# Optimization experiments

Hardware: AMD Instinct MI355X
Metric: run time of the kernel (lower is better)

The kernel has to match this reference:

```python
import jax, jax.numpy as jnp
import numpy as np

B, S, M, D, H = 2, 2048, 512, 1024, 16
HD = D // H      # head dim 64
KVC = D // 16    # MLA kv compression dim 64
QC = D // 32     # MLA q compression dim 32
RD = HD          # retrieval (qk) head dim 64
LOOKBACK = 8     # cross_window
EPS = 1e-6


def rmsnorm(x, w):
    return x * jax.lax.rsqrt(jnp.mean(x * x, axis=-1, keepdims=True) + EPS) * w


def setup_inputs():
    key = jax.random.key(0)
    ks = jax.random.split(key, 20)
    g = lambda i, shape: jax.random.normal(ks[i], shape, jnp.float32) * 0.02
    return {
        "x": jax.random.normal(ks[0], (B, S, D), jnp.float32),
        "memory": jax.random.normal(ks[1], (B, M, D), jnp.float32),
        "seg_ids": jnp.sort(jax.random.randint(ks[2], (B, S), 0, M), axis=-1),
        "norm1_w": jnp.ones((D,), jnp.float32),
        "W_dq": g(3, (D, QC)),
        "W_uq": g(4, (QC, H * RD)),
        "W_dkv": g(5, (D, KVC)),
        "W_uk": g(6, (KVC, H * RD)),
        "W_uv": g(7, (KVC, H * HD)),
        "W_o_self": g(8, (H * HD, D)),
        "norm2_w": jnp.ones((D,), jnp.float32),
        "W_q_c": g(9, (D, D)),
        "W_k_c": g(10, (D, D)),
        "W_v_c": g(11, (D, D)),
        "W_o_c": g(12, (D, D)),
        "norm3_w": jnp.ones((D,), jnp.float32),
        "W_gate": g(13, (D, 4 * D)),
        "W_up": g(14, (D, 4 * D)),
        "W_down": g(15, (4 * D, D)),
    }


def reference(x, memory, seg_ids, norm1_w, W_dq, W_uq, W_dkv, W_uk, W_uv,
              W_o_self, norm2_w, W_q_c, W_k_c, W_v_c, W_o_c, norm3_w,
              W_gate, W_up, W_down):
    # ---- MLA causal self-attention (low-rank compressed q/kv) ----
    h = rmsnorm(x, norm1_w)
    q = ((h @ W_dq) @ W_uq).reshape(B, S, H, RD)
    c_kv = h @ W_dkv                                  # [B,S,KVC]
    k = (c_kv @ W_uk).reshape(B, S, H, RD)
    v = (c_kv @ W_uv).reshape(B, S, H, HD)
    scores = jnp.einsum('bihd,bjhd->bhij', q, k) / np.float32(np.sqrt(RD))
    causal = jnp.tril(jnp.ones((S, S), bool))
    scores = jnp.where(causal, scores, -jnp.inf)
    attn = jax.nn.softmax(scores, axis=-1)
    o = jnp.einsum('bhij,bjhd->bihd', attn, v).reshape(B, S, H * HD)
    x = x + o @ W_o_self
    # ---- segment sliding-window cross-attention ----
    h = rmsnorm(x, norm2_w)
    qc = (h @ W_q_c).reshape(B, S, H, HD)
    kc = (memory @ W_k_c).reshape(B, M, H, HD)
    vc = (memory @ W_v_c).reshape(B, M, H, HD)
    sc = jnp.einsum('bihd,bjhd->bhij', qc, kc) / np.float32(np.sqrt(HD))
    kv_pos = jnp.arange(M)
    seg = seg_ids[:, :, None]                          # [B,S,1]
    allowed = (kv_pos[None, None, :] <= seg) & (kv_pos[None, None, :] >= seg - LOOKBACK)
    sc = jnp.where(allowed[:, None, :, :], sc, -jnp.inf)
    ac = jax.nn.softmax(sc, axis=-1)
    oc = jnp.einsum('bhij,bjhd->bihd', ac, vc).reshape(B, S, D)
    x = x + oc @ W_o_c
    # ---- SwiGLU FFN ----
    h = rmsnorm(x, norm3_w)
    x = x + (jax.nn.silu(h @ W_gate) * (h @ W_up)) @ W_down
    return x
```

## Files before the change

### kernel.cpp

```cpp
#include <hip/hip_runtime.h>
#include <stdint.h>

typedef unsigned short U16;
typedef __bf16 bf16x8 __attribute__((ext_vector_type(8)));
typedef unsigned short us8 __attribute__((ext_vector_type(8)));
typedef float f32x4 __attribute__((ext_vector_type(4)));

__device__ __forceinline__ U16 f2bf(float f) {
    unsigned u = __builtin_bit_cast(unsigned, f);
    unsigned r = (u + 0x7fff + ((u >> 16) & 1)) >> 16;
    return (U16)r;
}
__device__ __forceinline__ U16 f2bf_fast(float f) {
    return (U16)((__builtin_bit_cast(unsigned, f) + 0x8000u) >> 16);
}
__device__ __forceinline__ float bf2f(U16 v) {
    return __builtin_bit_cast(float, (unsigned)v << 16);
}
__device__ __forceinline__ bf16x8 ld8(const U16* p) { return __builtin_bit_cast(bf16x8, *(const us8*)p); }

__device__ __forceinline__ void async16(const U16* g, U16* l) {
    auto* gp = (const __attribute__((address_space(1))) U16*)g;
    auto* lp = (__attribute__((address_space(3))) U16*)(uintptr_t)(uint32_t)(uintptr_t)l;
    __builtin_amdgcn_global_load_lds(gp, lp, 16, 0, 0);
}

struct WEnt { const float* src; U16* dst; int K, N, Kpad, Npad, koff, noff, tiles; };
struct WTable { WEnt e[13]; };

__global__ __launch_bounds__(256) void wtrans_all(WTable t) {
    int bx = blockIdx.x, ei = 0;
    while (bx >= t.e[ei].tiles) { bx -= t.e[ei].tiles; ei++; }
    const WEnt E = t.e[ei];
    const int ntn = E.Npad >> 5;
    const int n0 = (bx % ntn) * 32, k0 = (bx / ntn) * 32;
    __shared__ float tile[32][33];
    const int tx = threadIdx.x & 31, ty = threadIdx.x >> 5;
#pragma unroll
    for (int i = 0; i < 4; i++) {
        int kk = k0 + ty + i * 8, n = n0 + tx;
        int k = kk - E.koff;
        float v = (k >= 0 && k < E.K && n < E.N) ? E.src[(size_t)k * E.N + n] : 0.f;
        tile[ty + i * 8][tx] = v;
    }
    __syncthreads();
#pragma unroll
    for (int i = 0; i < 4; i++) {
        int n = n0 + ty + i * 8, kk = k0 + tx;
        E.dst[(size_t)(E.noff + n) * E.Kpad + kk] = f2bf(tile[tx][ty + i * 8]);
    }
}

__global__ __launch_bounds__(256) void f2bf_k(const float* __restrict__ in, U16* __restrict__ out, int n) {
    int i = (blockIdx.x * 256 + threadIdx.x) * 4;
    if (i < n) {
        float4 v = *(const float4*)(in + i);
        out[i + 0] = f2bf(v.x); out[i + 1] = f2bf(v.y);
        out[i + 2] = f2bf(v.z); out[i + 3] = f2bf(v.w);
    }
}

__global__ __launch_bounds__(256) void cq_reduce(const float* __restrict__ p, U16* __restrict__ out) {
    int i = (blockIdx.x * 256 + threadIdx.x) * 4;
    const float4 a = *(const float4*)(p + i);
    const float4 b = *(const float4*)(p + 524288 + i);
    const float4 c = *(const float4*)(p + 2 * 524288 + i);
    const float4 d = *(const float4*)(p + 3 * 524288 + i);
    out[i + 0] = f2bf(a.x + b.x + c.x + d.x);
    out[i + 1] = f2bf(a.y + b.y + c.y + d.y);
    out[i + 2] = f2bf(a.z + b.z + c.z + d.z);
    out[i + 3] = f2bf(a.w + b.w + c.w + d.w);
}

__global__ __launch_bounds__(256) void rmsnorm_k(const float* __restrict__ x, const float* __restrict__ w,
                                                 U16* __restrict__ h) {
    const int row = blockIdx.x, tid = threadIdx.x;
    const float4 v = *(const float4*)(x + (size_t)row * 1024 + tid * 4);
    float ss = v.x * v.x + v.y * v.y + v.z * v.z + v.w * v.w;
#pragma unroll
    for (int o = 32; o > 0; o >>= 1) ss += __shfl_xor(ss, o);
    __shared__ float red[4];
    if ((tid & 63) == 0) red[tid >> 6] = ss;
    __syncthreads();
    float tot = red[0] + red[1] + red[2] + red[3];
    float sc = rsqrtf(tot * (1.0f / 1024.0f) + 1e-6f);
    const float4 wv = *(const float4*)(w + tid * 4);
    U16* hp = h + (size_t)row * 1024 + tid * 4;
    hp[0] = f2bf(v.x * sc * wv.x); hp[1] = f2bf(v.y * sc * wv.y);
    hp[2] = f2bf(v.z * sc * wv.z); hp[3] = f2bf(v.w * sc * wv.w);
}

__global__ __launch_bounds__(256) void qkuv_gemm(const U16* __restrict__ A, const U16* __restrict__ Wuqk,
                                                 const U16* __restrict__ Wuv,
                                                 U16* __restrict__ qkb, U16* __restrict__ vt) {
    __shared__ __align__(16) U16 As[2][128 * 32];
    __shared__ __align__(16) U16 Bs[2][128 * 32];
    __shared__ __align__(16) U16 Ts[4][64 * 80];
    const int tid = threadIdx.x;
    const bool isuv = blockIdx.x >= 16;
    const U16* Bt = isuv ? Wuv : Wuqk;
    const int n0 = (isuv ? blockIdx.x - 16 : blockIdx.x) * 128;
    const int m0 = blockIdx.y * 128;
    const int wave = tid >> 6, lane = tid & 63, l16 = lane & 15, quad = lane >> 4;
    const int wm = (wave >> 1) * 64, wn = (wave & 1) * 64;
    const int sr = lane >> 2, sc = (lane & 3) * 8;
    const U16* gA = A + (size_t)(m0 + wave * 32 + sr) * 128 + sc;
    const U16* gB = Bt + (size_t)(n0 + wave * 32 + sr) * 128 + sc;
    f32x4 acc[4][4] = {};
    for (int kt = 0; kt < 128; kt += 64) {
        __syncthreads();
#pragma unroll
        for (int p = 0; p < 2; p++) {
            const int o = kt + p * 32;
            async16(gA + o, &As[p][(wave * 32) * 32]);
            async16(gA + 16 * 128 + o, &As[p][(wave * 32 + 16) * 32]);
            async16(gB + o, &Bs[p][(wave * 32) * 32]);
            async16(gB + 16 * 128 + o, &Bs[p][(wave * 32 + 16) * 32]);
        }
        __syncthreads();
#pragma unroll
        for (int p = 0; p < 2; p++) {
            bf16x8 af[4], bfr[4];
#pragma unroll
            for (int i = 0; i < 4; i++) {
                af[i]  = ld8(&As[p][(wm + i * 16 + l16) * 32 + quad * 8]);
                bfr[i] = ld8(&Bs[p][(wn + i * 16 + l16) * 32 + quad * 8]);
            }
#pragma unroll
            for (int mi = 0; mi < 4; mi++)
#pragma unroll
                for (int ni = 0; ni < 4; ni++)
                    acc[mi][ni] = __builtin_amdgcn_mfma_f32_16x16x32_bf16(af[mi], bfr[ni], acc[mi][ni], 0, 0, 0);
        }
    }
    if (isuv) {
        U16* T = Ts[wave];
#pragma unroll
        for (int mi = 0; mi < 4; mi++)
#pragma unroll
            for (int ni = 0; ni < 4; ni++)
#pragma unroll
                for (int r = 0; r < 4; r++)
                    T[(ni * 16 + l16) * 80 + mi * 16 + quad * 4 + r] = f2bf(acc[mi][ni][r]);
#pragma unroll
        for (int c = 0; c < 8; c++) {
            int nloc = (lane >> 3) + 8 * c, mloc = (lane & 7) * 8;
            us8 v = *(const us8*)&T[nloc * 80 + mloc];
            *(us8*)&vt[(size_t)(n0 + wn + nloc) * 4096 + (m0 + wm + mloc)] = v;
        }
    } else {
#pragma unroll
        for (int mi = 0; mi < 4; mi++)
#pragma unroll
            for (int r = 0; r < 4; r++) {
                int m = m0 + wm + mi * 16 + quad * 4 + r;
#pragma unroll
                for (int ni = 0; ni < 4; ni++)
                    qkb[(size_t)m * 2048 + n0 + wn + ni * 16 + l16] = f2bf(acc[mi][ni][r]);
            }
    }
}

template <int EPI>
__global__ __launch_bounds__(256) void gemm_m64(const U16* __restrict__ A, const U16* __restrict__ Bt,
                                                void* __restrict__ Cout, const float* __restrict__ resid,
                                                int M, int N, int K, int lda, int ldb, int ldc) {
    __shared__ __align__(16) U16 As[4][64 * 32];
    __shared__ __align__(16) U16 Bs[4][128 * 32];
    const int tid = threadIdx.x;
    const int m0 = blockIdx.y * 64, n0 = blockIdx.x * 128;
    const int k0 = blockIdx.z * K;
    const int wave = tid >> 6, lane = tid & 63, l16 = lane & 15, quad = lane >> 4;
    const int wm = (wave >> 1) * 32, wn = (wave & 1) * 64;
    const int sr = lane >> 2, sc = (lane & 3) * 8;
    const U16* gA = A + (size_t)(m0 + wave * 16 + sr) * lda + sc + k0;
    const U16* gB = Bt + (size_t)(n0 + wave * 32 + sr) * ldb + sc + k0;
    f32x4 acc[2][4] = {};
    for (int kt = 0; kt < K; kt += 128) {
        __syncthreads();
#pragma unroll
        for (int p = 0; p < 4; p++) {
            const int o = kt + p * 32;
            async16(gA + o, &As[p][(wave * 16) * 32]);
            async16(gB + o, &Bs[p][(wave * 32) * 32]);
            async16(gB + (size_t)16 * ldb + o, &Bs[p][(wave * 32 + 16) * 32]);
        }
        __syncthreads();
#pragma unroll
        for (int p = 0; p < 4; p++) {
            bf16x8 af[2], bfr[4];
#pragma unroll
            for (int i = 0; i < 2; i++)
                af[i] = ld8(&As[p][(wm + i * 16 + l16) * 32 + quad * 8]);
#pragma unroll
            for (int i = 0; i < 4; i++)
                bfr[i] = ld8(&Bs[p][(wn + i * 16 + l16) * 32 + quad * 8]);
#pragma unroll
            for (int mi = 0; mi < 2; mi++)
#pragma unroll
                for (int ni = 0; ni < 4; ni++)
                    acc[mi][ni] = __builtin_amdgcn_mfma_f32_16x16x32_bf16(af[mi], bfr[ni], acc[mi][ni], 0, 0, 0);
        }
    }
#pragma unroll
    for (int mi = 0; mi < 2; mi++) {
#pragma unroll
        for (int r = 0; r < 4; r++) {
            int m = m0 + wm + mi * 16 + quad * 4 + r;
#pragma unroll
            for (int ni = 0; ni < 4; ni++) {
                int n = n0 + wn + ni * 16 + l16;
                float val = acc[mi][ni][r];
                if (EPI == 0) ((U16*)Cout)[(size_t)m * ldc + n] = f2bf(val);
                else if (EPI == 1) ((float*)Cout)[(size_t)m * ldc + n] = resid[(size_t)m * ldc + n] + val;
                else if (EPI == 5) ((float*)Cout)[(size_t)blockIdx.z * 524288 + (size_t)m * ldc + n] = val;
            }
        }
    }
}

__global__ __launch_bounds__(256) void qckv_gemm(const U16* __restrict__ hbuf, const U16* __restrict__ Wqc,
                                                 const U16* __restrict__ memb, const U16* __restrict__ Wkvc,
                                                 U16* __restrict__ qcb, U16* __restrict__ kvcb) {
    __shared__ __align__(16) U16 As[4][64 * 32];
    __shared__ __align__(16) U16 Bs[4][128 * 32];
    const int tid = threadIdx.x, bid = blockIdx.x;
    const U16 *A, *Bt; U16* C; int m0, n0, ldc;
    if (bid < 512) { A = hbuf; Bt = Wqc;  C = qcb;  m0 = (bid >> 3) * 64; n0 = (bid & 7) * 128;  ldc = 1024; }
    else { int b2 = bid - 512; A = memb; Bt = Wkvc; C = kvcb; m0 = (b2 >> 4) * 64; n0 = (b2 & 15) * 128; ldc = 2048; }
    const int wave = tid >> 6, lane = tid & 63, l16 = lane & 15, quad = lane >> 4;
    const int wm = (wave >> 1) * 32, wn = (wave & 1) * 64;
    const int sr = lane >> 2, sc = (lane & 3) * 8;
    const U16* gA = A + (size_t)(m0 + wave * 16 + sr) * 1024 + sc;
    const U16* gB = Bt + (size_t)(n0 + wave * 32 + sr) * 1024 + sc;
    f32x4 acc[2][4] = {};
    for (int kt = 0; kt < 1024; kt += 128) {
        __syncthreads();
#pragma unroll
        for (int p = 0; p < 4; p++) {
            const int o = kt + p * 32;
            async16(gA + o, &As[p][(wave * 16) * 32]);
            async16(gB + o, &Bs[p][(wave * 32) * 32]);
            async16(gB + 16 * 1024 + o, &Bs[p][(wave * 32 + 16) * 32]);
        }
        __syncthreads();
#pragma unroll
        for (int p = 0; p < 4; p++) {
            bf16x8 af[2], bfr[4];
#pragma unroll
            for (int i = 0; i < 2; i++)
                af[i] = ld8(&As[p][(wm + i * 16 + l16) * 32 + quad * 8]);
#pragma unroll
            for (int i = 0; i < 4; i++)
                bfr[i] = ld8(&Bs[p][(wn + i * 16 + l16) * 32 + quad * 8]);
#pragma unroll
            for (int mi = 0; mi < 2; mi++)
#pragma unroll
                for (int ni = 0; ni < 4; ni++)
                    acc[mi][ni] = __builtin_amdgcn_mfma_f32_16x16x32_bf16(af[mi], bfr[ni], acc[mi][ni], 0, 0, 0);
        }
    }
#pragma unroll
    for (int mi = 0; mi < 2; mi++)
#pragma unroll
        for (int r = 0; r < 4; r++) {
            int m = m0 + wm + mi * 16 + quad * 4 + r;
#pragma unroll
            for (int ni = 0; ni < 4; ni++)
                C[(size_t)m * ldc + n0 + wn + ni * 16 + l16] = f2bf(acc[mi][ni][r]);
        }
}

__global__ __launch_bounds__(512, 2) void ffn1_8ph(const U16* __restrict__ A, const U16* __restrict__ Wgu,
                                                   U16* __restrict__ Cout) {
    __shared__ __align__(16) U16 As[2][256 * 64];
    __shared__ __align__(16) U16 Bs[2][256 * 64];
    const int tid = threadIdx.x;
    const int wid = tid >> 6, lane = tid & 63;
    const int l16 = lane & 15, quad = lane >> 4;
    const int n0 = blockIdx.x * 128;
    const int m0 = blockIdx.y * 256;
    const int wr = wid >> 2, wc = wid & 3;
    const int wm = wr * 128;
    const int wn = wc * 64;
    const int srow = lane >> 3;
    const int schunk = (lane & 7) ^ srow;
    const U16* gA = A + (size_t)(m0 + wid * 32 + srow) * 1024 + schunk * 8;
    const U16* gB = Wgu + (size_t)((wid & 1) * 4096 + n0 + (wid >> 1) * 32 + srow) * 1024 + schunk * 8;

    auto STAGE = [&](int buf, int kt) {
        U16* la = &As[buf][(wid * 32) * 64];
        U16* lb = &Bs[buf][(wid * 32) * 64];
        const U16* pa = gA + kt;
        const U16* pb = gB + kt;
#pragma unroll
        for (int j = 0; j < 4; ++j) {
            async16(pa + j * 8 * 1024, la + j * 8 * 64);
            async16(pb + j * 8 * 1024, lb + j * 8 * 64);
        }
    };

    f32x4 acc[8][4] = {};

    auto TILE = [&](int buf) {
        const U16* Ab = &As[buf][0];
        const U16* Bb = &Bs[buf][0];
        const int cx = l16 & 7;
        bf16x8 a0[4][2], a1[4][2], b0[2][2], b1[2][2];
#pragma unroll
        for (int mi = 0; mi < 4; ++mi)
#pragma unroll
            for (int kh = 0; kh < 2; ++kh)
                a0[mi][kh] = ld8(&Ab[(wm + mi * 16 + l16) * 64 + (((kh * 4 + quad) ^ cx) << 3)]);
#pragma unroll
        for (int ni = 0; ni < 2; ++ni)
#pragma unroll
            for (int kh = 0; kh < 2; ++kh)
                b0[ni][kh] = ld8(&Bb[(wn + ni * 16 + l16) * 64 + (((kh * 4 + quad) ^ cx) << 3)]);
#pragma unroll
        for (int ni = 0; ni < 2; ++ni)
#pragma unroll
            for (int kh = 0; kh < 2; ++kh)
                b1[ni][kh] = ld8(&Bb[(wn + 32 + ni * 16 + l16) * 64 + (((kh * 4 + quad) ^ cx) << 3)]);
        __builtin_amdgcn_s_setprio(1);
#pragma unroll
        for (int mi = 0; mi < 4; ++mi)
#pragma unroll
            for (int ni = 0; ni < 2; ++ni)
#pragma unroll
                for (int kh = 0; kh < 2; ++kh)
                    acc[mi][ni] = __builtin_amdgcn_mfma_f32_16x16x32_bf16(a0[mi][kh], b0[ni][kh], acc[mi][ni], 0, 0, 0);
        __builtin_amdgcn_s_setprio(0);
#pragma unroll
        for (int mi = 0; mi < 4; ++mi)
#pragma unroll
            for (int kh = 0; kh < 2; ++kh)
                a1[mi][kh] = ld8(&Ab[(wm + 64 + mi * 16 + l16) * 64 + (((kh * 4 + quad) ^ cx) << 3)]);
        __builtin_amdgcn_s_setprio(1);
#pragma unroll
        for (int mi = 0; mi < 4; ++mi)
#pragma unroll
            for (int ni = 0; ni < 2; ++ni)
#pragma unroll
                for (int kh = 0; kh < 2; ++kh)
                    acc[mi][2 + ni] = __builtin_amdgcn_mfma_f32_16x16x32_bf16(a0[mi][kh], b1[ni][kh], acc[mi][2 + ni], 0, 0, 0);
        __builtin_amdgcn_s_setprio(0);
        __builtin_amdgcn_s_setprio(1);
#pragma unroll
        for (int mi = 0; mi < 4; ++mi)
#pragma unroll
            for (int ni = 0; ni < 2; ++ni)
#pragma unroll
                for (int kh = 0; kh < 2; ++kh)
                    acc[4 + mi][2 + ni] = __builtin_amdgcn_mfma_f32_16x16x32_bf16(a1[mi][kh], b1[ni][kh], acc[4 + mi][2 + ni], 0, 0, 0);
        __builtin_amdgcn_s_setprio(0);
        __builtin_amdgcn_s_setprio(1);
#pragma unroll
        for (int mi = 0; mi < 4; ++mi)
#pragma unroll
            for (int ni = 0; ni < 2; ++ni)
#pragma unroll
                for (int kh = 0; kh < 2; ++kh)
                    acc[4 + mi][ni] = __builtin_amdgcn_mfma_f32_16x16x32_bf16(a1[mi][kh], b0[ni][kh], acc[4 + mi][ni], 0, 0, 0);
        __builtin_amdgcn_s_setprio(0);
    };

    STAGE(0, 0);
    STAGE(1, 64);
#pragma unroll 1
    for (int t2 = 0; t2 < 7; ++t2) {
        asm volatile("s_waitcnt vmcnt(8)" ::: "memory");
        __builtin_amdgcn_s_barrier();
        __builtin_amdgcn_sched_barrier(0);
        TILE(0);
        __builtin_amdgcn_s_barrier();
        STAGE(0, (2 * t2 + 2) * 64);
        asm volatile("s_waitcnt vmcnt(8)" ::: "memory");
        __builtin_amdgcn_s_barrier();
        __builtin_amdgcn_sched_barrier(0);
        TILE(1);
        __builtin_amdgcn_s_barrier();
        STAGE(1, (2 * t2 + 3) * 64);
    }
    asm volatile("s_waitcnt vmcnt(8)" ::: "memory");
    __builtin_amdgcn_s_barrier();
    __builtin_amdgcn_sched_barrier(0);
    TILE(0);
    asm volatile("s_waitcnt vmcnt(0)" ::: "memory");
    __builtin_amdgcn_s_barrier();
    __builtin_amdgcn_sched_barrier(0);
    TILE(1);

#pragma unroll
    for (int mi = 0; mi < 8; ++mi)
#pragma unroll
        for (int r = 0; r < 4; ++r) {
            int m = m0 + wm + mi * 16 + quad * 4 + r;
#pragma unroll
            for (int ni = 0; ni < 2; ++ni) {
                int col = n0 + wc * 32 + ni * 16 + l16;
                float g = acc[mi][ni][r], u = acc[mi][ni + 2][r];
                float act = g / (1.f + __expf(-g)) * u;
                Cout[(size_t)m * 4096 + col] = f2bf(act);
            }
        }
}

__global__ __launch_bounds__(256, 3) void flash_self4(const U16* __restrict__ QK, const U16* __restrict__ Vt,
                                                      U16* __restrict__ Og) {
    __shared__ __align__(16) U16 Ks[2][32 * 64];
    __shared__ __align__(16) U16 Vs[2][64 * 32];
    __shared__ __align__(16) U16 Ps[4][1280];
    const int wave = threadIdx.x >> 6, lane = threadIdx.x & 63;
    const int l16 = lane & 15, quad = lane >> 4;
    const int bx = blockIdx.x;
    const int T = 15 - (bx >> 5);
    const int bh = bx & 31, b = bh >> 4, h = bh & 15;
    const int q0 = T * 128;
    const int NT = 4 * T + 4;
    const int G0 = q0 + wave * 16, G1 = q0 + 64 + wave * 16;
    bf16x8 aq[2][2];
    {
        const size_t r0 = (size_t)(b * 2048 + G0 + l16) * 2048 + h * 64;
        const size_t r1 = (size_t)(b * 2048 + G1 + l16) * 2048 + h * 64;
        aq[0][0] = ld8(QK + r0 + quad * 8); aq[0][1] = ld8(QK + r0 + 32 + quad * 8);
        aq[1][0] = ld8(QK + r1 + quad * 8); aq[1][1] = ld8(QK + r1 + 32 + quad * 8);
    }
    const int krow = wave * 8 + (lane >> 3);
    const int kchunk = (lane & 7) ^ (lane >> 3);
    const U16* gK = QK + (size_t)(b * 2048 + krow) * 2048 + 1024 + h * 64 + kchunk * 8;
    const int vrow = wave * 16 + (lane >> 2);
    const int vchunk = (lane & 3) ^ ((lane >> 2) & 3) ^ ((lane >> 4) & 3);
    const U16* gV = Vt + (size_t)(h * 64 + vrow) * 4096 + b * 2048 + vchunk * 8;

    auto STAGE = [&](int buf, int j0) {
        async16(gK + (size_t)j0 * 2048, &Ks[buf][(wave * 8) * 64]);
        async16(gV + j0, &Vs[buf][(wave * 16) * 32]);
    };

    f32x4 o[2][4] = {};
    float ls[2][4] = {};
    U16* Pw = Ps[wave];
    const int prd = l16 * 40 + ((quad ^ (l16 >> 2)) << 3);

    auto TILE = [&](int buf, int j0) {
        bf16x8 kf[2][2];
#pragma unroll
        for (int jh = 0; jh < 2; ++jh)
#pragma unroll
            for (int kh = 0; kh < 2; ++kh)
                kf[jh][kh] = ld8(&Ks[buf][(jh * 16 + l16) * 64 + (((kh * 4 + quad) ^ (l16 & 7)) << 3)]);
        bf16x8 vf[4];
#pragma unroll
        for (int dg = 0; dg < 4; ++dg)
            vf[dg] = ld8(&Vs[buf][(dg * 16 + l16) * 32 + ((quad ^ (l16 & 3) ^ ((l16 >> 2) & 3)) << 3)]);
#pragma unroll
        for (int g = 0; g < 2; ++g) {
            const int G = g ? G1 : G0;
            if (j0 < G + 16) {
                f32x4 s0 = {}, s1 = {};
                __builtin_amdgcn_s_setprio(1);
                s0 = __builtin_amdgcn_mfma_f32_16x16x32_bf16(aq[g][0], kf[0][0], s0, 0, 0, 0);
                s0 = __builtin_amdgcn_mfma_f32_16x16x32_bf16(aq[g][1], kf[0][1], s0, 0, 0, 0);
                s1 = __builtin_amdgcn_mfma_f32_16x16x32_bf16(aq[g][0], kf[1][0], s1, 0, 0, 0);
                s1 = __builtin_amdgcn_mfma_f32_16x16x32_bf16(aq[g][1], kf[1][1], s1, 0, 0, 0);
                __builtin_amdgcn_s_setprio(0);
                float p0[4], p1[4];
                if (j0 + 32 > G) {
#pragma unroll
                    for (int r = 0; r < 4; ++r) {
                        int qg = G + quad * 4 + r;
                        p0[r] = (j0 + l16 <= qg) ? __expf(fminf(s0[r] * 0.125f, 30.f)) : 0.f;
                        p1[r] = (j0 + 16 + l16 <= qg) ? __expf(fminf(s1[r] * 0.125f, 30.f)) : 0.f;
                    }
                } else {
#pragma unroll
                    for (int r = 0; r < 4; ++r) {
                        p0[r] = __expf(fminf(s0[r] * 0.125f, 30.f));
                        p1[r] = __expf(fminf(s1[r] * 0.125f, 30.f));
                    }
                }
#pragma unroll
                for (int r = 0; r < 4; ++r) {
                    ls[g][r] += p0[r] + p1[r];
                    int row = quad * 4 + r;
                    Pw[g * 640 + row * 40 + ((((l16 >> 3) + 0) ^ quad) << 3) + (l16 & 7)] = f2bf_fast(p0[r]);
                    Pw[g * 640 + row * 40 + ((((l16 >> 3) + 2) ^ quad) << 3) + (l16 & 7)] = f2bf_fast(p1[r]);
                }
                bf16x8 ap = ld8(&Pw[g * 640 + prd]);
                __builtin_amdgcn_s_setprio(1);
                o[g][0] = __builtin_amdgcn_mfma_f32_16x16x32_bf16(ap, vf[0], o[g][0], 0, 0, 0);
                o[g][1] = __builtin_amdgcn_mfma_f32_16x16x32_bf16(ap, vf[1], o[g][1], 0, 0, 0);
                o[g][2] = __builtin_amdgcn_mfma_f32_16x16x32_bf16(ap, vf[2], o[g][2], 0, 0, 0);
                o[g][3] = __builtin_amdgcn_mfma_f32_16x16x32_bf16(ap, vf[3], o[g][3], 0, 0, 0);
                __builtin_amdgcn_s_setprio(0);
            }
        }
    };

    STAGE(0, 0);
    STAGE(1, 32);
#pragma unroll 1
    for (int it = 0; it < NT - 2; ++it) {
        asm volatile("s_waitcnt vmcnt(2)" ::: "memory");
        __builtin_amdgcn_s_barrier();
        __builtin_amdgcn_sched_barrier(0);
        TILE(it & 1, it * 32);
        __builtin_amdgcn_s_barrier();
        STAGE(it & 1, (it + 2) * 32);
    }
    asm volatile("s_waitcnt vmcnt(2)" ::: "memory");
    __builtin_amdgcn_s_barrier();
    __builtin_amdgcn_sched_barrier(0);
    TILE(NT & 1, (NT - 2) * 32);
    asm volatile("s_waitcnt vmcnt(0)" ::: "memory");
    __builtin_amdgcn_s_barrier();
    __builtin_amdgcn_sched_barrier(0);
    TILE((NT - 1) & 1, (NT - 1) * 32);

#pragma unroll
    for (int g = 0; g < 2; ++g) {
        const int G = g ? G1 : G0;
#pragma unroll
        for (int r = 0; r < 4; ++r) {
            float v = ls[g][r];
            v += __shfl_xor(v, 1); v += __shfl_xor(v, 2);
            v += __shfl_xor(v, 4); v += __shfl_xor(v, 8);
            float inv = 1.0f / v;
            int qrow = G + quad * 4 + r;
            U16* op = Og + (size_t)(b * 2048 + qrow) * 1024 + h * 64 + l16;
#pragma unroll
            for (int dg = 0; dg < 4; ++dg)
                op[dg * 16] = f2bf(o[g][dg][r] * inv);
        }
    }
}

__global__ __launch_bounds__(256) void cross_attn(const U16* __restrict__ qc, const U16* __restrict__ kvc,
                                                  const int* __restrict__ seg_ids, U16* __restrict__ oc) {
    const int tok = blockIdx.x;
    const int b = tok >> 11;
    const int w = threadIdx.x >> 6, lane = threadIdx.x & 63;
    const int h = blockIdx.y * 4 + w;
    const int seg = seg_ids[tok];
    const size_t qoff = (size_t)tok * 1024 + h * 64 + lane;
    float q = bf2f(qc[qoff]);
    float s[9];
#pragma unroll
    for (int jj = 0; jj < 9; jj++) {
        int j = seg - 8 + jj;
        float sc = -INFINITY;
        if (j >= 0) {
            float kv = bf2f(kvc[((size_t)(b * 512) + j) * 2048 + h * 64 + lane]);
            sc = q * kv;
            sc += __shfl_xor(sc, 1); sc += __shfl_xor(sc, 2); sc += __shfl_xor(sc, 4);
            sc += __shfl_xor(sc, 8); sc += __shfl_xor(sc, 16); sc += __shfl_xor(sc, 32);
            sc *= 0.125f;
        }
        s[jj] = sc;
    }
    float m = s[0];
#pragma unroll
    for (int jj = 1; jj < 9; jj++) m = fmaxf(m, s[jj]);
    float l = 0.f, o = 0.f;
#pragma unroll
    for (int jj = 0; jj < 9; jj++) {
        int j = seg - 8 + jj;
        if (j >= 0) {
            float p = __expf(s[jj] - m);
            l += p;
            o += p * bf2f(kvc[((size_t)(b * 512) + j) * 2048 + 1024 + h * 64 + lane]);
        }
    }
    oc[qoff] = f2bf(o / l);
}

extern "C" void kernel_launch(void* const* d_in, const int* in_sizes, int n_in,
                              void* d_out, int out_size, void* d_ws, size_t ws_size,
                              hipStream_t stream) {
    const float* x      = (const float*)d_in[0];
    const float* memory = (const float*)d_in[1];
    const int*   seg    = (const int*)d_in[2];
    const float* n1w    = (const float*)d_in[3];
    const float* W_dq   = (const float*)d_in[4];
    const float* W_uq   = (const float*)d_in[5];
    const float* W_dkv  = (const float*)d_in[6];
    const float* W_uk   = (const float*)d_in[7];
    const float* W_uv   = (const float*)d_in[8];
    const float* W_os   = (const float*)d_in[9];
    const float* n2w    = (const float*)d_in[10];
    const float* W_qc   = (const float*)d_in[11];
    const float* W_kc   = (const float*)d_in[12];
    const float* W_vc   = (const float*)d_in[13];
    const float* W_oc   = (const float*)d_in[14];
    const float* n3w    = (const float*)d_in[15];
    const float* W_gate = (const float*)d_in[16];
    const float* W_up   = (const float*)d_in[17];
    const float* W_down = (const float*)d_in[18];
    (void)in_sizes; (void)n_in; (void)out_size; (void)ws_size;

    char* ws = (char*)d_ws;
    size_t off = 0;
    auto alloc = [&](size_t bytes) -> void* {
        void* p = ws + off;
        off += (bytes + 255) & ~(size_t)255;
        return p;
    };
    const size_t MB = 1024 * 1024;
    U16* hbuf     = (U16*)alloc(8 * MB);
    float* x1     = (float*)alloc(16 * MB);
    float* x2     = (float*)alloc(16 * MB);
    float* cq32   = (float*)alloc(8 * MB);
    U16* Wt_dqkv  = (U16*)alloc(128 * 1024 * 2);
    U16* Wt_uqk   = (U16*)alloc(2048 * 128 * 2);
    U16* Wt_uv    = (U16*)alloc(1024 * 128 * 2);
    U16* Wt_os    = (U16*)alloc(1024 * 1024 * 2);
    U16* Wt_qc    = (U16*)alloc(1024 * 1024 * 2);
    U16* Wt_kvc   = (U16*)alloc((size_t)2048 * 1024 * 2);
    U16* Wt_oc    = (U16*)alloc(1024 * 1024 * 2);
    U16* Wt_gu    = (U16*)alloc((size_t)8192 * 1024 * 2);
    U16* Wt_down  = (U16*)alloc((size_t)1024 * 4096 * 2);
    U16* mem_bf   = (U16*)alloc(1024 * 1024 * 2);
    char* arena   = ws + off;
    U16* cq  = (U16*)(arena);
    U16* qkb = (U16*)(arena + 1 * MB);
    U16* vt  = (U16*)(arena + 17 * MB);
    U16* ob  = (U16*)(arena + 25 * MB);
    U16* qcb  = (U16*)(arena);
    U16* kvcb = (U16*)(arena + 8 * MB);
    U16* ocb  = (U16*)(arena + 12 * MB);
    U16* gact = (U16*)(arena);

    WTable T;
    int i = 0;
    auto ent = [&](const float* s, U16* d, int K, int N, int Kpad, int Npad, int koff, int noff) {
        T.e[i++] = WEnt{s, d, K, N, Kpad, Npad, koff, noff, (Kpad >> 5) * (Npad >> 5)};
    };
    ent(W_dq,   Wt_dqkv, 1024, 32,   1024, 32,   0,  0);
    ent(W_dkv,  Wt_dqkv, 1024, 64,   1024, 96,   0,  32);
    ent(W_uq,   Wt_uqk,  32,   1024, 128,  1024, 0,  0);
    ent(W_uk,   Wt_uqk,  64,   1024, 128,  1024, 32, 1024);
    ent(W_uv,   Wt_uv,   64,   1024, 128,  1024, 32, 0);
    ent(W_os,   Wt_os,   1024, 1024, 1024, 1024, 0,  0);
    ent(W_qc,   Wt_qc,   1024, 1024, 1024, 1024, 0,  0);
    ent(W_kc,   Wt_kvc,  1024, 1024, 1024, 1024, 0,  0);
    ent(W_vc,   Wt_kvc,  1024, 1024, 1024, 1024, 0,  1024);
    ent(W_oc,   Wt_oc,   1024, 1024, 1024, 1024, 0,  0);
    ent(W_gate, Wt_gu,   1024, 4096, 1024, 4096, 0,  0);
    ent(W_up,   Wt_gu,   1024, 4096, 1024, 4096, 0,  4096);
    ent(W_down, Wt_down, 4096, 1024, 4096, 1024, 0,  0);
    int total_tiles = 0;
    for (int j = 0; j < 13; j++) total_tiles += T.e[j].tiles;
    wtrans_all<<<total_tiles, 256, 0, stream>>>(T);
    f2bf_k<<<1024, 256, 0, stream>>>(memory, mem_bf, 1024 * 1024);

    rmsnorm_k<<<4096, 256, 0, stream>>>(x, n1w, hbuf);
    gemm_m64<5><<<dim3(1, 64, 4), 256, 0, stream>>>(hbuf, Wt_dqkv, cq32, nullptr, 4096, 128, 256, 1024, 1024, 128);
    cq_reduce<<<512, 256, 0, stream>>>(cq32, cq);
    qkuv_gemm<<<dim3(24, 32), 256, 0, stream>>>(cq, Wt_uqk, Wt_uv, qkb, vt);
    flash_self4<<<512, 256, 0, stream>>>(qkb, vt, ob);
    gemm_m64<1><<<dim3(8, 64), 256, 0, stream>>>(ob, Wt_os, x1, x, 4096, 1024, 1024, 1024, 1024, 1024);

    rmsnorm_k<<<4096, 256, 0, stream>>>(x1, n2w, hbuf);
    qckv_gemm<<<768, 256, 0, stream>>>(hbuf, Wt_qc, mem_bf, Wt_kvc, qcb, kvcb);
    cross_attn<<<dim3(4096, 4), 256, 0, stream>>>(qcb, kvcb, seg, ocb);
    gemm_m64<1><<<dim3(8, 64), 256, 0, stream>>>(ocb, Wt_oc, x2, x1, 4096, 1024, 1024, 1024, 1024, 1024);

    rmsnorm_k<<<4096, 256, 0, stream>>>(x2, n3w, hbuf);
    ffn1_8ph<<<dim3(32, 16), 512, 0, stream>>>(hbuf, Wt_gu, gact);
    gemm_m64<1><<<dim3(8, 64), 256, 0, stream>>>(gact, Wt_down, (float*)d_out, x2, 4096, 1024, 4096, 4096, 4096, 1024);
}
```

Baseline: 499.6 us.

## Double-buffer async LDS staging in m64 GEMMs to overlap loads with MFMA

Rewrites the K-loop of gemm_m64 and qckv_gemm from a load-all-then-compute pattern over 128-wide K tiles into a two-stage ping-pong pipeline over 64-wide K tiles. The next tile is prefetched with async global-to-LDS loads while the current one feeds MFMAs, with explicit vmcnt waits and raw barriers. This is meant to hide global load latency that previously stalled each iteration. It uses the same LDS footprint but runs more iterations, and it relies on hand-counted vmcnt values that assume exactly six outstanding loads per stage.

```diff
diff --git a/kernel.cpp b/kernel.cpp
--- a/kernel.cpp
+++ b/kernel.cpp
@@ -165,8 +165,8 @@
 __global__ __launch_bounds__(256) void gemm_m64(const U16* __restrict__ A, const U16* __restrict__ Bt,
                                                 void* __restrict__ Cout, const float* __restrict__ resid,
                                                 int M, int N, int K, int lda, int ldb, int ldc) {
-    __shared__ __align__(16) U16 As[4][64 * 32];
-    __shared__ __align__(16) U16 Bs[4][128 * 32];
+    __shared__ __align__(16) U16 As[2][2][64 * 32];
+    __shared__ __align__(16) U16 Bs[2][2][128 * 32];
     const int tid = threadIdx.x;
     const int m0 = blockIdx.y * 64, n0 = blockIdx.x * 128;
     const int k0 = blockIdx.z * K;
@@ -175,32 +175,45 @@
     const int sr = lane >> 2, sc = (lane & 3) * 8;
     const U16* gA = A + (size_t)(m0 + wave * 16 + sr) * lda + sc + k0;
     const U16* gB = Bt + (size_t)(n0 + wave * 32 + sr) * ldb + sc + k0;
+
+    auto STAGE = [&](int buf, int kt) {
+#pragma unroll
+        for (int p = 0; p < 2; p++) {
+            const int o = kt + p * 32;
+            async16(gA + o, &As[buf][p][(wave * 16) * 32]);
+            async16(gB + o, &Bs[buf][p][(wave * 32) * 32]);
+            async16(gB + (size_t)16 * ldb + o, &Bs[buf][p][(wave * 32 + 16) * 32]);
+        }
+    };
+
     f32x4 acc[2][4] = {};
-    for (int kt = 0; kt < K; kt += 128) {
-        __syncthreads();
-#pragma unroll
-        for (int p = 0; p < 4; p++) {
-            const int o = kt + p * 32;
-            async16(gA + o, &As[p][(wave * 16) * 32]);
-            async16(gB + o, &Bs[p][(wave * 32) * 32]);
-            async16(gB + (size_t)16 * ldb + o, &Bs[p][(wave * 32 + 16) * 32]);
-        }
-        __syncthreads();
-#pragma unroll
-        for (int p = 0; p < 4; p++) {
+    const int NTK = K >> 6;
+    STAGE(0, 0);
+    STAGE(1, 64);
+#pragma unroll 1
+    for (int t = 0; t < NTK; ++t) {
+        if (t == NTK - 1) asm volatile("s_waitcnt vmcnt(0)" ::: "memory");
+        else              asm volatile("s_waitcnt vmcnt(6)" ::: "memory");
+        __builtin_amdgcn_s_barrier();
+        __builtin_amdgcn_sched_barrier(0);
+        const int buf = t & 1;
+#pragma unroll
+        for (int p = 0; p < 2; p++) {
             bf16x8 af[2], bfr[4];
 #pragma unroll
             for (int i = 0; i < 2; i++)
-                af[i] = ld8(&As[p][(wm + i * 16 + l16) * 32 + quad * 8]);
+                af[i] = ld8(&As[buf][p][(wm + i * 16 + l16) * 32 + quad * 8]);
 #pragma unroll
             for (int i = 0; i < 4; i++)
-                bfr[i] = ld8(&Bs[p][(wn + i * 16 + l16) * 32 + quad * 8]);
+                bfr[i] = ld8(&Bs[buf][p][(wn + i * 16 + l16) * 32 + quad * 8]);
 #pragma unroll
             for (int mi = 0; mi < 2; mi++)
 #pragma unroll
                 for (int ni = 0; ni < 4; ni++)
                     acc[mi][ni] = __builtin_amdgcn_mfma_f32_16x16x32_bf16(af[mi], bfr[ni], acc[mi][ni], 0, 0, 0);
         }
+        __builtin_amdgcn_s_barrier();
+        if (t + 2 < NTK) STAGE(buf, (t + 2) * 64);
     }
 #pragma unroll
     for (int mi = 0; mi < 2; mi++) {
@@ -222,8 +235,8 @@
 __global__ __launch_bounds__(256) void qckv_gemm(const U16* __restrict__ hbuf, const U16* __restrict__ Wqc,
                                                  const U16* __restrict__ memb, const U16* __restrict__ Wkvc,
                                                  U16* __restrict__ qcb, U16* __restrict__ kvcb) {
-    __shared__ __align__(16) U16 As[4][64 * 32];
-    __shared__ __align__(16) U16 Bs[4][128 * 32];
+    __shared__ __align__(16) U16 As[2][2][64 * 32];
+    __shared__ __align__(16) U16 Bs[2][2][128 * 32];
     const int tid = threadIdx.x, bid = blockIdx.x;
     const U16 *A, *Bt; U16* C; int m0, n0, ldc;
     if (bid < 512) { A = hbuf; Bt = Wqc;  C = qcb;  m0 = (bid >> 3) * 64; n0 = (bid & 7) * 128;  ldc = 1024; }
@@ -233,32 +246,44 @@
     const int sr = lane >> 2, sc = (lane & 3) * 8;
     const U16* gA = A + (size_t)(m0 + wave * 16 + sr) * 1024 + sc;
     const U16* gB = Bt + (size_t)(n0 + wave * 32 + sr) * 1024 + sc;
+
+    auto STAGE = [&](int buf, int kt) {
+#pragma unroll
+        for (int p = 0; p < 2; p++) {
+            const int o = kt + p * 32;
+            async16(gA + o, &As[buf][p][(wave * 16) * 32]);
+            async16(gB + o, &Bs[buf][p][(wave * 32) * 32]);
+            async16(gB + 16 * 1024 + o, &Bs[buf][p][(wave * 32 + 16) * 32]);
+        }
+    };
+
     f32x4 acc[2][4] = {};
-    for (int kt = 0; kt < 1024; kt += 128) {
-        __syncthreads();
-#pragma unroll
-        for (int p = 0; p < 4; p++) {
-            const int o = kt + p * 32;
-            async16(gA + o, &As[p][(wave * 16) * 32]);
-            async16(gB + o, &Bs[p][(wave * 32) * 32]);
-            async16(gB + 16 * 1024 + o, &Bs[p][(wave * 32 + 16) * 32]);
-        }
-        __syncthreads();
-#pragma unroll
-        for (int p = 0; p < 4; p++) {
+    STAGE(0, 0);
+    STAGE(1, 64);
+#pragma unroll 1
+    for (int t = 0; t < 16; ++t) {
+        if (t == 15) asm volatile("s_waitcnt vmcnt(0)" ::: "memory");
+        else         asm volatile("s_waitcnt vmcnt(6)" ::: "memory");
+        __builtin_amdgcn_s_barrier();
+        __builtin_amdgcn_sched_barrier(0);
+        const int buf = t & 1;
+#pragma unroll
+        for (int p = 0; p < 2; p++) {
             bf16x8 af[2], bfr[4];
 #pragma unroll
             for (int i = 0; i < 2; i++)
-                af[i] = ld8(&As[p][(wm + i * 16 + l16) * 32 + quad * 8]);
+                af[i] = ld8(&As[buf][p][(wm + i * 16 + l16) * 32 + quad * 8]);
 #pragma unroll
             for (int i = 0; i < 4; i++)
-                bfr[i] = ld8(&Bs[p][(wn + i * 16 + l16) * 32 + quad * 8]);
+                bfr[i] = ld8(&Bs[buf][p][(wn + i * 16 + l16) * 32 + quad * 8]);
 #pragma unroll
             for (int mi = 0; mi < 2; mi++)
 #pragma unroll
                 for (int ni = 0; ni < 4; ni++)
                     acc[mi][ni] = __builtin_amdgcn_mfma_f32_16x16x32_bf16(af[mi], bfr[ni], acc[mi][ni], 0, 0, 0);
         }
+        __builtin_amdgcn_s_barrier();
+        if (t + 2 < 16) STAGE(buf, (t + 2) * 64);
     }
 #pragma unroll
     for (int mi = 0; mi < 2; mi++)
```

Result: no change. 499.6 us (-0.0%).
